# Performance work log

Measured on AMD Instinct MI355X. Metric: run time of the kernel, lower is better.

## Reference

```python
import jax, jax.numpy as jnp
import numpy as np
import math

IN_CH = 512
OUT_CH = 512
K = 3
STYLE_DIM = 512
B, H, W = 8, 64, 64


def setup_inputs() -> dict:
    key = jax.random.key(0)
    k1, k2, k3, k4 = jax.random.split(key, 4)
    return {
        "input": jax.random.normal(k1, (B, IN_CH, H, W), dtype=jnp.float32),
        "style": jax.random.normal(k2, (B, STYLE_DIM), dtype=jnp.float32),
        "weight": jax.random.normal(k3, (1, OUT_CH, IN_CH, K, K), dtype=jnp.float32),
        "mod_weight": jax.random.normal(k4, (IN_CH, STYLE_DIM), dtype=jnp.float32),
        "mod_bias": jnp.ones((IN_CH,), dtype=jnp.float32),
    }


def reference(input, style, weight, mod_weight, mod_bias):
    batch, in_ch, h, w = input.shape
    out_ch = weight.shape[1]
    k = weight.shape[-1]
    conv_scale = 1.0 / math.sqrt(in_ch * k * k)
    lin_scale = 1.0 / math.sqrt(STYLE_DIM)  # EqualLinear scale, lr_mul=1

    # modulation: EqualLinear(style_dim -> in_channel), bias_init=1, no activation
    s = style @ (mod_weight * lin_scale).T + mod_bias  # [B, Cin]

    # per-sample modulated weight: [B, Cout, Cin, K, K]
    wmod = conv_scale * weight * s[:, None, :, None, None]
    demod = jax.lax.rsqrt(jnp.sum(wmod * wmod, axis=(2, 3, 4)) + 1e-8)  # [B, Cout]
    wmod = wmod * demod[:, :, None, None, None]

    # grouped conv with groups = batch (exactly mirrors the torch path)
    lhs = input.reshape(1, batch * in_ch, h, w)
    rhs = wmod.reshape(batch * out_ch, in_ch, k, k)
    pad = (k - 1) // 2
    out = jax.lax.conv_general_dilated(
        lhs, rhs,
        window_strides=(1, 1),
        padding=[(pad, pad), (pad, pad)],
        dimension_numbers=("NCHW", "OIHW", "NCHW"),
        feature_group_count=batch,
    )
    return out.reshape(batch, out_ch, h, w)
```

## Files before the change

### kernel.cpp

```cpp
#include <hip/hip_runtime.h>
#include <hip/hip_bf16.h>
#include <stdint.h>

typedef __attribute__((ext_vector_type(8))) short bf16x8;
typedef __attribute__((ext_vector_type(4))) float f32x4;
typedef __attribute__((ext_vector_type(8))) unsigned short u16x8;

__device__ __forceinline__ unsigned short f2bf(float f) {
  unsigned int u = __float_as_uint(f);
  u = u + 0x7fffu + ((u >> 16) & 1u);
  return (unsigned short)(u >> 16);
}

__global__ void k1(const float* __restrict__ w, const float* __restrict__ style,
                   const float* __restrict__ mw, const float* __restrict__ mb,
                   unsigned short* __restrict__ wp, float* __restrict__ s,
                   float* __restrict__ wsq) {
  const int bid = blockIdx.x, t = threadIdx.x;
  if (bid < 1152) {
    const int id = bid * 256 + t;
    const int c8 = id & 7, o = (id >> 3) & 511, cb = (id >> 12) & 7, kk = id >> 15;
    const int ci0 = cb*64 + c8*8;
    u16x8 h;
    #pragma unroll
    for (int e = 0; e < 8; ++e) h[e] = f2bf(w[((size_t)(o*512 + ci0 + e))*9 + kk]);
    char* base = (char*)wp + (((size_t)kk*8 + cb)*512 + o)*128
               + ((unsigned)(c8*16) ^ (unsigned)((o & 7) << 4));
    *(u16x8*)base = h;
  } else if (bid < 1160) {
    __shared__ float st[512];
    const int b = bid - 1152;
    st[t]       = style[b*512 + t];
    st[t + 256] = style[b*512 + t + 256];
    __syncthreads();
    for (int k = 0; k < 2; ++k) {
      int c = t + k*256;
      const float* row = mw + (size_t)c * 512;
      float acc = 0.f;
      for (int j = 0; j < 512; ++j) acc += st[j] * row[j];
      s[b*512 + c] = acc * 0.04419417382415922f + mb[c];
    }
  } else {
    int g = (bid - 1160) * 256 + t;
    const float* p = w + (size_t)g * 9;
    float acc = 0.f;
    #pragma unroll
    for (int q = 0; q < 9; ++q) { float v = p[q]; acc += v*v; }
    wsq[g] = acc;
  }
}

__global__ void k_demod(const float* __restrict__ s, const float* __restrict__ wsq,
                        float* __restrict__ dm) {
  __shared__ float s2[512];
  const int g = blockIdx.x * 256 + threadIdx.x;
  const int b = g >> 9, o = g & 511, t = threadIdx.x;
  float v0 = s[b*512 + t], v1 = s[b*512 + t + 256];
  s2[t] = v0*v0; s2[t+256] = v1*v1;
  __syncthreads();
  const float* row = wsq + (size_t)o * 512;
  float acc = 0.f;
  for (int j = 0; j < 512; ++j) acc += s2[j] * row[j];
  dm[g] = 0.014731391274719739f * rsqrtf(acc * (1.0f/4608.0f) + 1e-8f);
}

__global__ void k_inprep(const float* __restrict__ in, const float* __restrict__ s,
                         unsigned short* __restrict__ ib) {
  __shared__ __align__(16) unsigned char lds[32768];
  const int tid = threadIdx.x;
  const int x = tid & 63, c8 = tid >> 6;
  const int yq = blockIdx.x, cb = blockIdx.y, b = blockIdx.z;
  const int ci0 = cb*64 + c8*8;
  f32x4 s0 = *(const f32x4*)(s + b*512 + ci0);
  f32x4 s1 = *(const f32x4*)(s + b*512 + ci0 + 4);
  const float* p = in + (((size_t)b*512 + ci0) * 64 + yq*4) * 64 + x;
  u16x8 h[4];
  #pragma unroll
  for (int j = 0; j < 4; ++j) {
    #pragma unroll
    for (int e = 0; e < 4; ++e) h[j][e]     = f2bf(p[(size_t)e*4096 + j*64] * s0[e]);
    #pragma unroll
    for (int e = 0; e < 4; ++e) h[j][e + 4] = f2bf(p[(size_t)(e+4)*4096 + j*64] * s1[e]);
  }
  const unsigned so = (unsigned)(x*128) + (((unsigned)(c8*16)) ^ ((unsigned)(x & 7) << 4));
  #pragma unroll
  for (int j = 0; j < 4; ++j)
    *(u16x8*)(lds + j*8192 + so) = h[j];
  __syncthreads();
  const int rx = tid >> 3, rc = tid & 7;
  const unsigned ro = (unsigned)(rx*128) + (((unsigned)(rc*16)) ^ ((unsigned)(rx & 7) << 4));
  unsigned short* dst = ib + (((size_t)(b*8 + cb)*64 + yq*4) * 4096) + tid*8;
  #pragma unroll
  for (int j = 0; j < 4; ++j)
    *(u16x8*)(dst + j*4096) = *(const u16x8*)(lds + j*8192 + ro);
}

__global__ __launch_bounds__(512, 2) void k_conv(const unsigned short* __restrict__ ib,
                                                 const unsigned short* __restrict__ wp,
                                                 const float* __restrict__ dm,
                                                 float* __restrict__ out) {
  __shared__ __align__(16) unsigned char ldsA[3*32768];
  __shared__ __align__(16) unsigned char ldsB[49152];

  const int tid = threadIdx.x;
  const int lan15 = tid & 15;
  const int lgrp = (tid >> 4) & 3;
  const int wid = tid >> 6;
  const int wm = wid >> 2, wn = wid & 3;
  const unsigned wg = blockIdx.x;
  const int b = wg & 7, pt = (wg >> 3) & 15, ot = (wg >> 7) & 1;
  const int o0 = ot * 256, y0 = pt * 4;

  const unsigned short* ibb = ib + (size_t)b * 8 * 64 * 64 * 64;

  auto stageA = [&](int tap, int cbb, int buf) {
    const char* src = (const char*)(wp + (((size_t)tap*8 + cbb)*512 + (size_t)o0) * 64);
    unsigned char* dst = ldsA + buf*32768;
    #pragma unroll
    for (int r = 0; r < 4; ++r) {
      __builtin_amdgcn_global_load_lds(
        (const __attribute__((address_space(1))) unsigned int*)(src + tid*16 + r*8192),
        (__attribute__((address_space(3))) unsigned int*)(dst + tid*16 + r*8192),
        16, 0, 0);
    }
  };

  u16x8 bv[6];
  auto loadB = [&](int cbb) {
    const int c8 = tid & 7, x = (tid >> 3) & 63;
    const unsigned short* base = ibb + ((size_t)cbb * 64 * 64 + (size_t)x) * 64 + c8*8;
    #pragma unroll
    for (int j = 0; j < 6; ++j) {
      const int yi = y0 - 1 + j;
      const int yc = yi < 0 ? 0 : (yi > 63 ? 63 : yi);
      bv[j] = *(const u16x8*)(base + (size_t)yc * 4096);
    }
  };
  auto writeB = [&]() {
    const int c8 = tid & 7, x = (tid >> 3) & 63;
    const unsigned off = (unsigned)(x*128) + (((unsigned)(c8*16)) ^ ((unsigned)(x & 7) << 4));
    #pragma unroll
    for (int j = 0; j < 6; ++j) {
      const int yi = y0 - 1 + j;
      const bool valid = (yi >= 0) & (yi < 64);
      u16x8 v = valid ? bv[j] : (u16x8){0,0,0,0,0,0,0,0};
      *(u16x8*)(ldsB + j*8192 + off) = v;
    }
  };

  f32x4 acc[8][4];
  #pragma unroll
  for (int mf = 0; mf < 8; ++mf)
    #pragma unroll
    for (int nf = 0; nf < 4; ++nf)
      acc[mf][nf] = (f32x4){0.f, 0.f, 0.f, 0.f};

  const int aB0 = (wm*128 + lan15)*128 + ((lgrp*16) ^ ((lan15 & 7) << 4));
  const int aB1 = aB0 ^ 64;
  int cB0[3], cB1[3];
  #pragma unroll
  for (int kx = 0; kx < 3; ++kx) {
    const int x0 = lan15 + kx - 1;
    cB0[kx] = wn*8192 + x0*128 + ((lgrp*16) ^ ((x0 & 7) << 4));
    cB1[kx] = cB0[kx] ^ 64;
  }
  const bool zL = (lan15 == 0), zR = (lan15 == 15);

#define BARR asm volatile("s_barrier" ::: "memory")
#define GATE(N) asm volatile("s_waitcnt vmcnt(" #N ")\n\ts_barrier" ::: "memory")

#define RD_A(MH, KS) _Pragma("unroll") \
    for (int i = 0; i < 4; ++i) \
      af[i] = *(const bf16x8*)(Ab + ((KS) ? aB1 : aB0) + ((MH)*4 + i)*2048);

#define RD_B(KS) _Pragma("unroll") \
    for (int nf = 0; nf < 4; ++nf) { \
      bf16x8 v = *(const bf16x8*)(Bb + ((KS) ? cB1[kx_] : cB0[kx_]) + nf*2048); \
      if (kx_ == 0 && nf == 0) { if (zL) v = (bf16x8){0,0,0,0,0,0,0,0}; } \
      if (kx_ == 2 && nf == 3) { if (zR) v = (bf16x8){0,0,0,0,0,0,0,0}; } \
      bfr[nf] = v; }

#define MF16(MH) { __builtin_amdgcn_s_setprio(1); \
    _Pragma("unroll") for (int i = 0; i < 4; ++i) \
      _Pragma("unroll") for (int nf = 0; nf < 4; ++nf) \
        acc[(MH)*4+i][nf] = __builtin_amdgcn_mfma_f32_16x16x32_bf16(af[i], bfr[nf], acc[(MH)*4+i][nf], 0, 0, 0); \
    __builtin_amdgcn_s_setprio(0); }

#define PH4 \
    RD_A(0,0) RD_B(0) MF16(0) \
    RD_A(1,0) BARR; MF16(1) \
    RD_A(0,1) RD_B(1) BARR; MF16(0) \
    RD_A(1,1) BARR; MF16(1)

#define TAP(KK) { \
    constexpr int ky_ = (KK)/3, kx_ = (KK)%3; \
    const unsigned char* Ab = ldsA + ((KK)%3)*32768; \
    const unsigned char* Bb = ldsB + ky_*8192; \
    bf16x8 af[4], bfr[4]; \
    stageA((KK)+2, cb, ((KK)+2)%3); \
    GATE(8); \
    PH4 }

  loadB(0);
  asm volatile("" ::: "memory");
  stageA(0, 0, 0);
  stageA(1, 0, 1);
  asm volatile("s_waitcnt vmcnt(8)" ::: "memory");
  writeB();
  asm volatile("s_waitcnt vmcnt(4) lgkmcnt(0)\n\ts_barrier" ::: "memory");

  for (int cb = 0; cb < 7; ++cb) {
    TAP(0) TAP(1) TAP(2) TAP(3) TAP(4) TAP(5) TAP(6)
    {
      constexpr int ky_ = 2, kx_ = 1;
      const unsigned char* Ab = ldsA + (7%3)*32768;
      const unsigned char* Bb = ldsB + ky_*8192;
      bf16x8 af[4], bfr[4];
      stageA(0, cb + 1, 0);
      GATE(8);
      loadB(cb + 1);
      PH4
    }
    {
      asm volatile("s_waitcnt vmcnt(0)" ::: "memory");
      stageA(1, cb + 1, 1);
      constexpr int ky_ = 2, kx_ = 2;
      const unsigned char* Ab = ldsA + (8%3)*32768;
      const unsigned char* Bb = ldsB + ky_*8192;
      bf16x8 af[4], bfr[4];
      PH4
      BARR;
      writeB();
      asm volatile("s_waitcnt lgkmcnt(0)\n\ts_barrier" ::: "memory");
    }
  }
  {
    const int cb = 7;
    TAP(0) TAP(1) TAP(2) TAP(3) TAP(4) TAP(5) TAP(6)
    {
      constexpr int ky_ = 2, kx_ = 1;
      const unsigned char* Ab = ldsA + (7%3)*32768;
      const unsigned char* Bb = ldsB + ky_*8192;
      bf16x8 af[4], bfr[4];
      GATE(4);
      PH4
    }
    {
      asm volatile("s_waitcnt vmcnt(0)" ::: "memory");
      constexpr int ky_ = 2, kx_ = 2;
      const unsigned char* Ab = ldsA + (8%3)*32768;
      const unsigned char* Bb = ldsB + ky_*8192;
      bf16x8 af[4], bfr[4];
      PH4
    }
  }

  const float* dmb = dm + b*512;
  float* outb = out + (size_t)b * 512 * 4096;
  #pragma unroll
  for (int mf = 0; mf < 8; ++mf) {
    asm volatile("" ::: "memory");
    const int o = o0 + wm*128 + mf*16 + lgrp*4;
    const f32x4 d4 = *(const f32x4*)(dmb + o);
    #pragma unroll
    for (int nf = 0; nf < 4; ++nf) {
      const int p = pt*256 + wn*64 + nf*16 + lan15;
      #pragma unroll
      for (int r = 0; r < 4; ++r)
        outb[(size_t)(o + r) * 4096 + p] = acc[mf][nf][r] * d4[r];
    }
  }
#undef TAP
#undef PH4
#undef MF16
#undef RD_B
#undef RD_A
#undef GATE
#undef BARR
}

extern "C" void kernel_launch(void* const* d_in, const int* in_sizes, int n_in,
                              void* d_out, int out_size, void* d_ws, size_t ws_size,
                              hipStream_t stream) {
  const float* input  = (const float*)d_in[0];
  const float* style  = (const float*)d_in[1];
  const float* weight = (const float*)d_in[2];
  const float* mw     = (const float*)d_in[3];
  const float* mb     = (const float*)d_in[4];
  float* out = (float*)d_out;
  char* ws = (char*)d_ws;
  float* s     = (float*)ws;
  float* dm    = (float*)(ws + 16384);
  float* wsq   = (float*)(ws + 32768);
  unsigned short* wp = (unsigned short*)(ws + 1081344);
  unsigned short* ib = (unsigned short*)(ws + 5799936);

  hipLaunchKernelGGL(k1,       dim3(2184),      dim3(256), 0, stream, weight, style, mw, mb, wp, s, wsq);
  hipLaunchKernelGGL(k_demod,  dim3(16),        dim3(256), 0, stream, s, wsq, dm);
  hipLaunchKernelGGL(k_inprep, dim3(16, 8, 8),  dim3(512), 0, stream, input, s, ib);
  hipLaunchKernelGGL(k_conv,   dim3(256),       dim3(512), 0, stream, ib, wp, dm, out);
}
```

Measured before the change: 187.8 us.

## Merge preprocessing kernels and read each weight row once for packing and norms

Weight packing now has each thread load all nine taps for eight input channels together, convert them into nine swizzled bf16 vectors, and compute the sum of squares from the same registers. This drops the strided per-tap rereads and the separate wsq pass. The demodulation and input-prep kernels are merged into one launch, cutting the kernel count from four to three. The cost is much higher register use per thread in k1, and 128 blocks gives low parallelism for the packing work.

```diff
diff --git a/kernel.cpp b/kernel.cpp
--- a/kernel.cpp
+++ b/kernel.cpp
@@ -17,19 +17,34 @@
                    unsigned short* __restrict__ wp, float* __restrict__ s,
                    float* __restrict__ wsq) {
   const int bid = blockIdx.x, t = threadIdx.x;
-  if (bid < 1152) {
+  if (bid < 128) {
     const int id = bid * 256 + t;
-    const int c8 = id & 7, o = (id >> 3) & 511, cb = (id >> 12) & 7, kk = id >> 15;
+    const int c8 = id & 7, o = (id >> 3) & 511, cb = id >> 12;
     const int ci0 = cb*64 + c8*8;
-    u16x8 h;
-    #pragma unroll
-    for (int e = 0; e < 8; ++e) h[e] = f2bf(w[((size_t)(o*512 + ci0 + e))*9 + kk]);
-    char* base = (char*)wp + (((size_t)kk*8 + cb)*512 + o)*128
-               + ((unsigned)(c8*16) ^ (unsigned)((o & 7) << 4));
-    *(u16x8*)base = h;
-  } else if (bid < 1160) {
+    const float* p = w + ((size_t)(o*512 + ci0)) * 9;
+    float v[8][9];
+    #pragma unroll
+    for (int e = 0; e < 8; ++e)
+      #pragma unroll
+      for (int kk = 0; kk < 9; ++kk) v[e][kk] = p[e*9 + kk];
+    #pragma unroll
+    for (int e = 0; e < 8; ++e) {
+      float acc = 0.f;
+      #pragma unroll
+      for (int kk = 0; kk < 9; ++kk) acc += v[e][kk] * v[e][kk];
+      wsq[(size_t)o*512 + ci0 + e] = acc;
+    }
+    const unsigned sw = (unsigned)(c8*16) ^ (unsigned)((o & 7) << 4);
+    #pragma unroll
+    for (int kk = 0; kk < 9; ++kk) {
+      u16x8 h;
+      #pragma unroll
+      for (int e = 0; e < 8; ++e) h[e] = f2bf(v[e][kk]);
+      *(u16x8*)((char*)wp + (((size_t)kk*8 + cb)*512 + o)*128 + sw) = h;
+    }
+  } else {
     __shared__ float st[512];
-    const int b = bid - 1152;
+    const int b = bid - 128;
     st[t]       = style[b*512 + t];
     st[t + 256] = style[b*512 + t + 256];
     __syncthreads();
@@ -40,59 +55,52 @@
       for (int j = 0; j < 512; ++j) acc += st[j] * row[j];
       s[b*512 + c] = acc * 0.04419417382415922f + mb[c];
     }
+  }
+}
+
+__global__ void k2(const float* __restrict__ in, const float* __restrict__ s,
+                   const float* __restrict__ wsq, float* __restrict__ dm,
+                   unsigned short* __restrict__ ib) {
+  const int bid = blockIdx.x, tid = threadIdx.x;
+  if (bid < 8) {
+    __shared__ float s2[512];
+    const int b = bid, o = tid;
+    float v = s[b*512 + tid];
+    s2[tid] = v * v;
+    __syncthreads();
+    const float* row = wsq + (size_t)o * 512;
+    float acc = 0.f;
+    for (int j = 0; j < 512; ++j) acc += s2[j] * row[j];
+    dm[b*512 + o] = 0.014731391274719739f * rsqrtf(acc * (1.0f/4608.0f) + 1e-8f);
   } else {
-    int g = (bid - 1160) * 256 + t;
-    const float* p = w + (size_t)g * 9;
-    float acc = 0.f;
-    #pragma unroll
-    for (int q = 0; q < 9; ++q) { float v = p[q]; acc += v*v; }
-    wsq[g] = acc;
-  }
-}
-
-__global__ void k_demod(const float* __restrict__ s, const float* __restrict__ wsq,
-                        float* __restrict__ dm) {
-  __shared__ float s2[512];
-  const int g = blockIdx.x * 256 + threadIdx.x;
-  const int b = g >> 9, o = g & 511, t = threadIdx.x;
-  float v0 = s[b*512 + t], v1 = s[b*512 + t + 256];
-  s2[t] = v0*v0; s2[t+256] = v1*v1;
-  __syncthreads();
-  const float* row = wsq + (size_t)o * 512;
-  float acc = 0.f;
-  for (int j = 0; j < 512; ++j) acc += s2[j] * row[j];
-  dm[g] = 0.014731391274719739f * rsqrtf(acc * (1.0f/4608.0f) + 1e-8f);
-}
-
-__global__ void k_inprep(const float* __restrict__ in, const float* __restrict__ s,
-                         unsigned short* __restrict__ ib) {
-  __shared__ __align__(16) unsigned char lds[32768];
-  const int tid = threadIdx.x;
-  const int x = tid & 63, c8 = tid >> 6;
-  const int yq = blockIdx.x, cb = blockIdx.y, b = blockIdx.z;
-  const int ci0 = cb*64 + c8*8;
-  f32x4 s0 = *(const f32x4*)(s + b*512 + ci0);
-  f32x4 s1 = *(const f32x4*)(s + b*512 + ci0 + 4);
-  const float* p = in + (((size_t)b*512 + ci0) * 64 + yq*4) * 64 + x;
-  u16x8 h[4];
-  #pragma unroll
-  for (int j = 0; j < 4; ++j) {
-    #pragma unroll
-    for (int e = 0; e < 4; ++e) h[j][e]     = f2bf(p[(size_t)e*4096 + j*64] * s0[e]);
-    #pragma unroll
-    for (int e = 0; e < 4; ++e) h[j][e + 4] = f2bf(p[(size_t)(e+4)*4096 + j*64] * s1[e]);
-  }
-  const unsigned so = (unsigned)(x*128) + (((unsigned)(c8*16)) ^ ((unsigned)(x & 7) << 4));
-  #pragma unroll
-  for (int j = 0; j < 4; ++j)
-    *(u16x8*)(lds + j*8192 + so) = h[j];
-  __syncthreads();
-  const int rx = tid >> 3, rc = tid & 7;
-  const unsigned ro = (unsigned)(rx*128) + (((unsigned)(rc*16)) ^ ((unsigned)(rx & 7) << 4));
-  unsigned short* dst = ib + (((size_t)(b*8 + cb)*64 + yq*4) * 4096) + tid*8;
-  #pragma unroll
-  for (int j = 0; j < 4; ++j)
-    *(u16x8*)(dst + j*4096) = *(const u16x8*)(lds + j*8192 + ro);
+    __shared__ __align__(16) unsigned char lds[32768];
+    const int u = bid - 8;
+    const int yq = u & 15, cb = (u >> 4) & 7, b = u >> 7;
+    const int x = tid & 63, c8 = tid >> 6;
+    const int ci0 = cb*64 + c8*8;
+    f32x4 s0 = *(const f32x4*)(s + b*512 + ci0);
+    f32x4 s1 = *(const f32x4*)(s + b*512 + ci0 + 4);
+    const float* p = in + (((size_t)b*512 + ci0) * 64 + yq*4) * 64 + x;
+    u16x8 h[4];
+    #pragma unroll
+    for (int j = 0; j < 4; ++j) {
+      #pragma unroll
+      for (int e = 0; e < 4; ++e) h[j][e]     = f2bf(p[(size_t)e*4096 + j*64] * s0[e]);
+      #pragma unroll
+      for (int e = 0; e < 4; ++e) h[j][e + 4] = f2bf(p[(size_t)(e+4)*4096 + j*64] * s1[e]);
+    }
+    const unsigned so = (unsigned)(x*128) + (((unsigned)(c8*16)) ^ ((unsigned)(x & 7) << 4));
+    #pragma unroll
+    for (int j = 0; j < 4; ++j)
+      *(u16x8*)(lds + j*8192 + so) = h[j];
+    __syncthreads();
+    const int rx = tid >> 3, rc = tid & 7;
+    const unsigned ro = (unsigned)(rx*128) + (((unsigned)(rc*16)) ^ ((unsigned)(rx & 7) << 4));
+    unsigned short* dst = ib + (((size_t)(b*8 + cb)*64 + yq*4) * 4096) + tid*8;
+    #pragma unroll
+    for (int j = 0; j < 4; ++j)
+      *(u16x8*)(dst + j*4096) = *(const u16x8*)(lds + j*8192 + ro);
+  }
 }
 
 __global__ __launch_bounds__(512, 2) void k_conv(const unsigned short* __restrict__ ib,
@@ -295,8 +303,7 @@
   unsigned short* wp = (unsigned short*)(ws + 1081344);
   unsigned short* ib = (unsigned short*)(ws + 5799936);
 
-  hipLaunchKernelGGL(k1,       dim3(2184),      dim3(256), 0, stream, weight, style, mw, mb, wp, s, wsq);
-  hipLaunchKernelGGL(k_demod,  dim3(16),        dim3(256), 0, stream, s, wsq, dm);
-  hipLaunchKernelGGL(k_inprep, dim3(16, 8, 8),  dim3(512), 0, stream, input, s, ib);
-  hipLaunchKernelGGL(k_conv,   dim3(256),       dim3(512), 0, stream, ib, wp, dm, out);
-}
+  hipLaunchKernelGGL(k1,     dim3(136),  dim3(256), 0, stream, weight, style, mw, mb, wp, s, wsq);
+  hipLaunchKernelGGL(k2,     dim3(1032), dim3(512), 0, stream, input, s, wsq, dm, ib);
+  hipLaunchKernelGGL(k_conv, dim3(256),  dim3(512), 0, stream, ib, wp, dm, out);
+}
```

After: 194.4 us. 1.04x slower.

## Fuse input prep into conv kernel via cooperative grid sync

Applied to the files above, without the earlier changes.

Removes the separate k_inprep launch and has each conv workgroup convert its share of the input (scale by style, cast to bf16, transpose via LDS) before a grid-wide barrier, then runs the convolution. The launch becomes cooperative so all 256 workgroups are co-resident. This saves one kernel launch and its tail, but adds a grid sync, and the prep phase now runs on only 256 workgroups instead of 1024.

```diff
diff --git a/kernel.cpp b/kernel.cpp
--- a/kernel.cpp
+++ b/kernel.cpp
@@ -1,6 +1,9 @@
 #include <hip/hip_runtime.h>
 #include <hip/hip_bf16.h>
+#include <hip/hip_cooperative_groups.h>
 #include <stdint.h>
+
+namespace cg = cooperative_groups;
 
 typedef __attribute__((ext_vector_type(8))) short bf16x8;
 typedef __attribute__((ext_vector_type(4))) float f32x4;
@@ -64,40 +67,11 @@
   dm[g] = 0.014731391274719739f * rsqrtf(acc * (1.0f/4608.0f) + 1e-8f);
 }
 
-__global__ void k_inprep(const float* __restrict__ in, const float* __restrict__ s,
-                         unsigned short* __restrict__ ib) {
-  __shared__ __align__(16) unsigned char lds[32768];
-  const int tid = threadIdx.x;
-  const int x = tid & 63, c8 = tid >> 6;
-  const int yq = blockIdx.x, cb = blockIdx.y, b = blockIdx.z;
-  const int ci0 = cb*64 + c8*8;
-  f32x4 s0 = *(const f32x4*)(s + b*512 + ci0);
-  f32x4 s1 = *(const f32x4*)(s + b*512 + ci0 + 4);
-  const float* p = in + (((size_t)b*512 + ci0) * 64 + yq*4) * 64 + x;
-  u16x8 h[4];
-  #pragma unroll
-  for (int j = 0; j < 4; ++j) {
-    #pragma unroll
-    for (int e = 0; e < 4; ++e) h[j][e]     = f2bf(p[(size_t)e*4096 + j*64] * s0[e]);
-    #pragma unroll
-    for (int e = 0; e < 4; ++e) h[j][e + 4] = f2bf(p[(size_t)(e+4)*4096 + j*64] * s1[e]);
-  }
-  const unsigned so = (unsigned)(x*128) + (((unsigned)(c8*16)) ^ ((unsigned)(x & 7) << 4));
-  #pragma unroll
-  for (int j = 0; j < 4; ++j)
-    *(u16x8*)(lds + j*8192 + so) = h[j];
-  __syncthreads();
-  const int rx = tid >> 3, rc = tid & 7;
-  const unsigned ro = (unsigned)(rx*128) + (((unsigned)(rc*16)) ^ ((unsigned)(rx & 7) << 4));
-  unsigned short* dst = ib + (((size_t)(b*8 + cb)*64 + yq*4) * 4096) + tid*8;
-  #pragma unroll
-  for (int j = 0; j < 4; ++j)
-    *(u16x8*)(dst + j*4096) = *(const u16x8*)(lds + j*8192 + ro);
-}
-
-__global__ __launch_bounds__(512, 2) void k_conv(const unsigned short* __restrict__ ib,
+__global__ __launch_bounds__(512, 2) void k_conv(const float* __restrict__ in,
+                                                 const float* __restrict__ s,
                                                  const unsigned short* __restrict__ wp,
                                                  const float* __restrict__ dm,
+                                                 unsigned short* ib,
                                                  float* __restrict__ out) {
   __shared__ __align__(16) unsigned char ldsA[3*32768];
   __shared__ __align__(16) unsigned char ldsB[49152];
@@ -110,6 +84,39 @@
   const unsigned wg = blockIdx.x;
   const int b = wg & 7, pt = (wg >> 3) & 15, ot = (wg >> 7) & 1;
   const int o0 = ot * 256, y0 = pt * 4;
+
+  {
+    const int x = tid & 63, c8 = tid >> 6;
+    const int rx = tid >> 3, rc = tid & 7;
+    const unsigned so = (unsigned)(x*128)  + (((unsigned)(c8*16)) ^ ((unsigned)(x  & 7) << 4));
+    const unsigned ro = (unsigned)(rx*128) + (((unsigned)(rc*16)) ^ ((unsigned)(rx & 7) << 4));
+    #pragma unroll
+    for (int q = 0; q < 4; ++q) {
+      const int cb = ot*4 + q;
+      const int ci0 = cb*64 + c8*8;
+      f32x4 s0 = *(const f32x4*)(s + b*512 + ci0);
+      f32x4 s1 = *(const f32x4*)(s + b*512 + ci0 + 4);
+      const float* p = in + (((size_t)b*512 + ci0) * 64 + y0) * 64 + x;
+      u16x8 h[4];
+      #pragma unroll
+      for (int j = 0; j < 4; ++j) {
+        #pragma unroll
+        for (int e = 0; e < 4; ++e) h[j][e]     = f2bf(p[(size_t)e*4096 + j*64] * s0[e]);
+        #pragma unroll
+        for (int e = 0; e < 4; ++e) h[j][e + 4] = f2bf(p[(size_t)(e+4)*4096 + j*64] * s1[e]);
+      }
+      #pragma unroll
+      for (int j = 0; j < 4; ++j)
+        *(u16x8*)(ldsA + j*8192 + so) = h[j];
+      __syncthreads();
+      unsigned short* dst = ib + (((size_t)(b*8 + cb)*64 + y0) * 4096) + tid*8;
+      #pragma unroll
+      for (int j = 0; j < 4; ++j)
+        *(u16x8*)(dst + j*4096) = *(const u16x8*)(ldsA + j*8192 + ro);
+      __syncthreads();
+    }
+  }
+  cg::this_grid().sync();
 
   const unsigned short* ibb = ib + (size_t)b * 8 * 64 * 64 * 64;
 
@@ -295,8 +302,9 @@
   unsigned short* wp = (unsigned short*)(ws + 1081344);
   unsigned short* ib = (unsigned short*)(ws + 5799936);
 
-  hipLaunchKernelGGL(k1,       dim3(2184),      dim3(256), 0, stream, weight, style, mw, mb, wp, s, wsq);
-  hipLaunchKernelGGL(k_demod,  dim3(16),        dim3(256), 0, stream, s, wsq, dm);
-  hipLaunchKernelGGL(k_inprep, dim3(16, 8, 8),  dim3(512), 0, stream, input, s, ib);
-  hipLaunchKernelGGL(k_conv,   dim3(256),       dim3(512), 0, stream, ib, wp, dm, out);
-}
+  hipLaunchKernelGGL(k1,      dim3(2184), dim3(256), 0, stream, weight, style, mw, mb, wp, s, wsq);
+  hipLaunchKernelGGL(k_demod, dim3(16),   dim3(256), 0, stream, s, wsq, dm);
+
+  void* args[] = {(void*)&input, (void*)&s, (void*)&wp, (void*)&dm, (void*)&ib, (void*)&out};
+  hipLaunchCooperativeKernel((const void*)k_conv, dim3(256), dim3(512), args, 0, stream);
+}
```

Result: slower. 239.7 us (+27.7%).
